# Performance work log

Hardware: AMD Instinct MI355X
Metric: run time of the kernel (lower is better)

Reference implementation:

```python
import jax, jax.numpy as jnp
import numpy as np

SEQ, BS, IN, HID, RANK = 512, 64, 1024, 1024, 256

def _xavier(key, shape):
    fan_in, fan_out = shape[0], shape[1]
    a = jnp.sqrt(6.0 / (fan_in + fan_out))
    return jax.random.uniform(key, shape, jnp.float32, -a, a)

def setup_inputs() -> dict:
    key = jax.random.key(0)
    ks = jax.random.split(key, 17)
    d = {"x": jax.random.normal(ks[0], (SEQ, BS, IN), jnp.float32)}
    names = ["ii", "hi", "if_", "hf", "ig", "hg", "io", "ho"]
    for i, n in enumerate(names):
        in_dim = IN if n[0] == "i" else HID
        d[f"W_{n}U"] = _xavier(ks[1 + 2 * i], (in_dim, RANK))
        d[f"W_{n}V"] = _xavier(ks[2 + 2 * i], (RANK, HID))
    d["b_i"] = jnp.zeros((HID,), jnp.float32)
    d["b_f"] = jnp.zeros((HID,), jnp.float32)
    d["b_g"] = jnp.zeros((HID,), jnp.float32)
    d["b_o"] = jnp.zeros((HID,), jnp.float32)
    return d

def reference(x, W_iiU, W_iiV, W_hiU, W_hiV, W_if_U, W_if_V, W_hfU, W_hfV,
              W_igU, W_igV, W_hgU, W_hgV, W_ioU, W_ioV, W_hoU, W_hoV,
              b_i, b_f, b_g, b_o):
    # Precompute input-side low-rank projections across all timesteps: (S,B,H)
    xi = (x @ W_iiU) @ W_iiV
    xf = (x @ W_if_U) @ W_if_V
    xg = (x @ W_igU) @ W_igV
    xo = (x @ W_ioU) @ W_ioV

    h0 = jnp.zeros((x.shape[1], b_i.shape[0]), x.dtype)
    c0 = jnp.zeros_like(h0)

    def step(carry, ins):
        h, c = carry
        xi_t, xf_t, xg_t, xo_t = ins
        i_t = jax.nn.sigmoid(xi_t + (h @ W_hiU) @ W_hiV + b_i)
        f_t = jax.nn.sigmoid(xf_t + (h @ W_hfU) @ W_hfV + b_f)
        g_t = jnp.tanh(xg_t + (h @ W_hgU) @ W_hgV + b_g)
        o_t = jax.nn.sigmoid(xo_t + (h @ W_hoU) @ W_hoV + b_o)
        c_n = f_t * c + i_t * g_t
        h_n = o_t * jnp.tanh(c_n)
        return (h_n, c_n), h_n

    (h_T, c_T), hidden_seq = jax.lax.scan(step, (h0, c0), (xi, xf, xg, xo))
    return hidden_seq, h_T, c_T
```

## Files before the change

### kernel.cpp

```cpp
#include <hip/hip_runtime.h>
#include <hip/hip_bf16.h>
#include <stdint.h>


typedef __attribute__((ext_vector_type(8))) short short8;
typedef __attribute__((ext_vector_type(4))) float f32x4;

#define MFMA16(a, b, c) __builtin_amdgcn_mfma_f32_16x16x32_bf16((a), (b), (c), 0, 0, 0)

__device__ inline unsigned short f2bf(float f) {
  union { float f; unsigned int u; } v; v.f = f;
  unsigned int r = v.u + 0x7fffu + ((v.u >> 16) & 1u);
  return (unsigned short)(r >> 16);
}
__device__ inline float bf2f(unsigned short u) {
  union { unsigned int u; float f; } v; v.u = ((unsigned int)u) << 16; return v.f;
}
__device__ inline float sigmoidf_(float x) {
  return 1.f / (1.f + __expf(-x));
}
__device__ inline float tanhf_(float x) {
  float cx = fminf(fmaxf(x, -15.f), 15.f);
  float e = __expf(2.f * cx);
  return (e - 1.f) / (e + 1.f);
}


__global__ __launch_bounds__(256) void convert_f32_bf16(
    const float* __restrict__ src, unsigned short* __restrict__ dst, int n) {
  int i = (blockIdx.x * 256 + threadIdx.x) * 4;
  if (i < n) {
    float4 v = *(const float4*)&src[i];
    ushort4 o;
    o.x = f2bf(v.x); o.y = f2bf(v.y); o.z = f2bf(v.z); o.w = f2bf(v.w);
    *(ushort4*)&dst[i] = o;
  }
}

__global__ __launch_bounds__(256) void transpose_f32_bf16(
    const float* __restrict__ src, unsigned short* __restrict__ dst, int R, int C) {
  int idx = blockIdx.x * 256 + threadIdx.x;
  if (idx < R * C) {
    int r = idx / C, c = idx - r * C;
    dst[(size_t)c * R + r] = f2bf(src[idx]);
  }
}


template <bool AF32>
__device__ inline short8 load_a8(const void* A, size_t row, int K, int k) {
  if constexpr (AF32) {
    const float* a = (const float*)A + row * (size_t)K + k;
    float4 f0 = *(const float4*)a;
    float4 f1 = *(const float4*)(a + 4);
    short8 r;
    r[0] = (short)f2bf(f0.x); r[1] = (short)f2bf(f0.y);
    r[2] = (short)f2bf(f0.z); r[3] = (short)f2bf(f0.w);
    r[4] = (short)f2bf(f1.x); r[5] = (short)f2bf(f1.y);
    r[6] = (short)f2bf(f1.z); r[7] = (short)f2bf(f1.w);
    return r;
  } else {
    return *(const short8*)((const unsigned short*)A + row * (size_t)K + k);
  }
}

template <bool AF32>
__global__ __launch_bounds__(256) void gemm_bf16(
    const void* __restrict__ A, const unsigned short* __restrict__ BT,
    unsigned short* __restrict__ C, int M, int N, int K,
    int ldc, int cstride, int coff) {
  __shared__ unsigned short As[128 * 64];
  __shared__ unsigned short Bs[128 * 64];

  const int tid = threadIdx.x;
  const int m0 = blockIdx.y * 128;
  const int n0 = blockIdx.x * 128;
  const int w = tid >> 6, l = tid & 63;
  const int wm = w >> 1, wn = w & 1;
  const int lr = l & 15, lk = (l >> 4) * 8;

  const int srow = tid >> 3;
  const int sseg = (tid & 7) * 8;

  f32x4 acc[4][4] = {};

  short8 av[4], bv[4];
#pragma unroll
  for (int p = 0; p < 4; ++p) {
    av[p] = load_a8<AF32>(A, m0 + p * 32 + srow, K, sseg);
    bv[p] = *(const short8*)(BT + (size_t)(n0 + p * 32 + srow) * K + sseg);
  }

  for (int k0 = 0; k0 < K; k0 += 64) {
    __syncthreads();
#pragma unroll
    for (int p = 0; p < 4; ++p) {
      *(short8*)&As[(p * 32 + srow) * 64 + sseg] = av[p];
      *(short8*)&Bs[(p * 32 + srow) * 64 + sseg] = bv[p];
    }
    __syncthreads();
    if (k0 + 64 < K) {
#pragma unroll
      for (int p = 0; p < 4; ++p) {
        av[p] = load_a8<AF32>(A, m0 + p * 32 + srow, K, k0 + 64 + sseg);
        bv[p] = *(const short8*)(BT + (size_t)(n0 + p * 32 + srow) * K + k0 + 64 + sseg);
      }
    }
#pragma unroll
    for (int kk = 0; kk < 2; ++kk) {
      const int ko = kk * 32 + lk;
      short8 a[4], b[4];
#pragma unroll
      for (int i = 0; i < 4; ++i)
        a[i] = *(const short8*)&As[(wm * 64 + i * 16 + lr) * 64 + ko];
#pragma unroll
      for (int j = 0; j < 4; ++j)
        b[j] = *(const short8*)&Bs[(wn * 64 + j * 16 + lr) * 64 + ko];
#pragma unroll
      for (int i = 0; i < 4; ++i)
#pragma unroll
        for (int j = 0; j < 4; ++j)
          acc[i][j] = MFMA16(a[i], b[j], acc[i][j]);
    }
  }

#pragma unroll
  for (int i = 0; i < 4; ++i) {
#pragma unroll
    for (int j = 0; j < 4; ++j) {
      const int rb = m0 + wm * 64 + i * 16 + (l >> 4) * 4;
      const int cb = n0 + wn * 64 + j * 16 + lr;
#pragma unroll
      for (int r = 0; r < 4; ++r)
        C[(size_t)(rb + r) * ldc + (size_t)cb * cstride + coff] = f2bf(acc[i][j][r]);
    }
  }
}


__global__ __launch_bounds__(256) void lstm_step(
    const unsigned short* __restrict__ Wrt,
    const unsigned short* __restrict__ xp_t,
    const unsigned short* __restrict__ hprev,
    unsigned short* __restrict__ hnext,
    const float* __restrict__ bi, const float* __restrict__ bf_,
    const float* __restrict__ bg, const float* __restrict__ bo,
    float* __restrict__ cstate,
    float* __restrict__ out_h,
    float* __restrict__ out_hT, float* __restrict__ out_cT,
    int t) {
  __shared__ float pre[64 * 64];

  const int tid = threadIdx.x;
  const int w = tid >> 6, l = tid & 63;
  const int c0 = blockIdx.x * 64;
  const int mr = (w >> 1) * 32;
  const int nc = c0 + (w & 1) * 32;
  const int lr = l & 15, lk = (l >> 4) * 8;

  f32x4 acc[2][2] = {};

  if (t > 0) {
#pragma unroll 2
    for (int k = 0; k < 1024; k += 32) {
      short8 a0 = *(const short8*)&hprev[(mr + lr) * 1024 + k + lk];
      short8 a1 = *(const short8*)&hprev[(mr + 16 + lr) * 1024 + k + lk];
      short8 b0 = *(const short8*)&Wrt[(size_t)(nc + lr) * 1024 + k + lk];
      short8 b1 = *(const short8*)&Wrt[(size_t)(nc + 16 + lr) * 1024 + k + lk];
      acc[0][0] = MFMA16(a0, b0, acc[0][0]);
      acc[0][1] = MFMA16(a0, b1, acc[0][1]);
      acc[1][0] = MFMA16(a1, b0, acc[1][0]);
      acc[1][1] = MFMA16(a1, b1, acc[1][1]);
    }
  }

#pragma unroll
  for (int i = 0; i < 2; ++i)
#pragma unroll
    for (int j = 0; j < 2; ++j)
#pragma unroll
      for (int r = 0; r < 4; ++r)
        pre[(mr + i * 16 + (l >> 4) * 4 + r) * 64 + (w & 1) * 32 + j * 16 + lr] =
            acc[i][j][r];
  __syncthreads();

#pragma unroll
  for (int rep = 0; rep < 4; ++rep) {
    const int cell = rep * 256 + tid;
    const int bb = cell >> 4;
    const int hh = cell & 15;
    const int hid = (c0 >> 2) + hh;

    float4 p = *(const float4*)&pre[bb * 64 + hh * 4];
    ushort4 xq = *(const ushort4*)&xp_t[bb * 4096 + c0 + hh * 4];

    float pi = p.x + bf2f(xq.x) + bi[hid];
    float pf = p.y + bf2f(xq.y) + bf_[hid];
    float pg = p.z + bf2f(xq.z) + bg[hid];
    float po = p.w + bf2f(xq.w) + bo[hid];

    float ig = sigmoidf_(pi);
    float fg = sigmoidf_(pf);
    float gg = tanhf_(pg);
    float og = sigmoidf_(po);

    float cold = (t == 0) ? 0.f : cstate[bb * 1024 + hid];
    float cn = fg * cold + ig * gg;
    float hn = og * tanhf_(cn);

    cstate[bb * 1024 + hid] = cn;
    out_h[bb * 1024 + hid] = hn;
    hnext[bb * 1024 + hid] = f2bf(hn);
    if (t == 511) {
      out_hT[bb * 1024 + hid] = hn;
      out_cT[bb * 1024 + hid] = cn;
    }
  }
}


extern "C" void kernel_launch(void* const* d_in, const int* in_sizes, int n_in,
                              void* d_out, int out_size, void* d_ws, size_t ws_size,
                              hipStream_t stream) {
  const float* x = (const float*)d_in[0];
  const float* WU[8]; const float* WV[8];
  for (int i = 0; i < 8; ++i) {
    WU[i] = (const float*)d_in[1 + 2 * i];
    WV[i] = (const float*)d_in[2 + 2 * i];
  }
  const int IGATE[4] = {0, 2, 4, 6};
  const int HGATE[4] = {1, 3, 5, 7};
  const float* bi = (const float*)d_in[17];
  const float* bf_ = (const float*)d_in[18];
  const float* bg = (const float*)d_in[19];
  const float* bo = (const float*)d_in[20];

  char* ws = (char*)d_ws;
  const size_t OFF_UTI = 0;
  const size_t OFF_VTI = OFF_UTI + 2097152;
  const size_t OFF_UBH = OFF_VTI + 2097152;
  const size_t OFF_VTH = OFF_UBH + 2097152;
  const size_t OFF_P   = OFF_VTH + 2097152;
  const size_t OFF_XP  = OFF_P + 16777216;
  const size_t OFF_WRT = OFF_XP + 268435456;
  const size_t OFF_HPP = OFF_WRT + 8388608;
  const size_t OFF_CST = OFF_HPP + 262144;

  unsigned short* uti = (unsigned short*)(ws + OFF_UTI);
  unsigned short* vti = (unsigned short*)(ws + OFF_VTI);
  unsigned short* ubh = (unsigned short*)(ws + OFF_UBH);
  unsigned short* vth = (unsigned short*)(ws + OFF_VTH);
  unsigned short* pbuf = (unsigned short*)(ws + OFF_P);
  unsigned short* xp = (unsigned short*)(ws + OFF_XP);
  unsigned short* wrt = (unsigned short*)(ws + OFF_WRT);
  unsigned short* hpp = (unsigned short*)(ws + OFF_HPP);
  float* cst = (float*)(ws + OFF_CST);
  float* out = (float*)d_out;

  for (int g = 0; g < 4; ++g) {
    transpose_f32_bf16<<<1024, 256, 0, stream>>>(WU[IGATE[g]], uti + g * 262144, 1024, 256);
    transpose_f32_bf16<<<1024, 256, 0, stream>>>(WV[IGATE[g]], vti + g * 262144, 256, 1024);
    convert_f32_bf16<<<256, 256, 0, stream>>>(WU[HGATE[g]], ubh + g * 262144, 262144);
    transpose_f32_bf16<<<1024, 256, 0, stream>>>(WV[HGATE[g]], vth + g * 262144, 256, 1024);
  }

  for (int g = 0; g < 4; ++g) {
    gemm_bf16<false><<<dim3(8, 8), 256, 0, stream>>>(
        vth + g * 262144, ubh + g * 262144, wrt,
        1024, 1024, 256, 4096, 1, g * 1024);
  }

  for (int g = 0; g < 4; ++g) {
    gemm_bf16<true><<<dim3(2, 256), 256, 0, stream>>>(
        x, uti + g * 262144, pbuf, 32768, 256, 1024, 256, 1, 0);
    gemm_bf16<false><<<dim3(8, 256), 256, 0, stream>>>(
        pbuf, vti + g * 262144, xp, 32768, 1024, 256, 4096, 4, g);
  }

  for (int t = 0; t < 512; ++t) {
    const unsigned short* hp = hpp + ((t & 1) ^ 1) * 65536;
    unsigned short* hn = hpp + (t & 1) * 65536;
    lstm_step<<<64, 256, 0, stream>>>(
        wrt, xp + (size_t)t * 262144, hp, hn,
        bi, bf_, bg, bo, cst,
        out + (size_t)t * 65536,
        out + 33554432, out + 33554432 + 65536, t);
  }
}
```

Baseline: 10.89 ms.

## Replace per-timestep LSTM launches with persistent kernel and grid barrier

Swaps the 512 per-step kernel launches for a single persistent kernel of 256 workgroups that loops over time and syncs through an atomic grid-wide barrier. Each workgroup keeps its slice of the recurrent weight matrix in registers, and the cell state stays in registers instead of going through global memory. The four waves split the K dimension and combine partial sums in shared memory. The goal is to remove launch overhead and the repeated weight reloads. In exchange, correctness depends on all 256 workgroups being resident at the same time, and the spin-wait barrier adds latency to every step.

```diff
diff --git a/kernel.cpp b/kernel.cpp
--- a/kernel.cpp
+++ b/kernel.cpp
@@ -45,6 +45,8 @@
     dst[(size_t)c * R + r] = f2bf(src[idx]);
   }
 }
+
+__global__ void zero_u32(unsigned int* p) { *p = 0u; }
 
 
 template <bool AF32>
@@ -138,83 +140,98 @@
 }
 
 
-__global__ __launch_bounds__(256) void lstm_step(
+#define NWG 256
+
+__global__ __launch_bounds__(256) void lstm_persistent(
     const unsigned short* __restrict__ Wrt,
-    const unsigned short* __restrict__ xp_t,
-    const unsigned short* __restrict__ hprev,
-    unsigned short* __restrict__ hnext,
+    const unsigned short* __restrict__ xp,
+    unsigned short* __restrict__ hpp,
     const float* __restrict__ bi, const float* __restrict__ bf_,
     const float* __restrict__ bg, const float* __restrict__ bo,
-    float* __restrict__ cstate,
-    float* __restrict__ out_h,
-    float* __restrict__ out_hT, float* __restrict__ out_cT,
-    int t) {
-  __shared__ float pre[64 * 64];
+    float* __restrict__ out,
+    unsigned int* __restrict__ bar) {
+  __shared__ float part[4][64][17];
 
   const int tid = threadIdx.x;
-  const int w = tid >> 6, l = tid & 63;
-  const int c0 = blockIdx.x * 64;
-  const int mr = (w >> 1) * 32;
-  const int nc = c0 + (w & 1) * 32;
-  const int lr = l & 15, lk = (l >> 4) * 8;
-
-  f32x4 acc[2][2] = {};
-
-  if (t > 0) {
-#pragma unroll 2
-    for (int k = 0; k < 1024; k += 32) {
-      short8 a0 = *(const short8*)&hprev[(mr + lr) * 1024 + k + lk];
-      short8 a1 = *(const short8*)&hprev[(mr + 16 + lr) * 1024 + k + lk];
-      short8 b0 = *(const short8*)&Wrt[(size_t)(nc + lr) * 1024 + k + lk];
-      short8 b1 = *(const short8*)&Wrt[(size_t)(nc + 16 + lr) * 1024 + k + lk];
-      acc[0][0] = MFMA16(a0, b0, acc[0][0]);
-      acc[0][1] = MFMA16(a0, b1, acc[0][1]);
-      acc[1][0] = MFMA16(a1, b0, acc[1][0]);
-      acc[1][1] = MFMA16(a1, b1, acc[1][1]);
-    }
-  }
-
-#pragma unroll
-  for (int i = 0; i < 2; ++i)
-#pragma unroll
-    for (int j = 0; j < 2; ++j)
+  const int w = tid >> 6;
+  const int l = tid & 63;
+  const int lr = l & 15;
+  const int lk = (l >> 4) * 8;
+  const int c0 = blockIdx.x * 16;
+  const int kbase = w * 256;
+
+  short8 bfrag[8];
+#pragma unroll
+  for (int kk = 0; kk < 8; ++kk)
+    bfrag[kk] = *(const short8*)&Wrt[(size_t)(c0 + lr) * 1024 + kbase + kk * 32 + lk];
+
+  const int bb = tid >> 2;
+  const int hh = tid & 3;
+  const int hid = (c0 >> 2) + hh;
+  const float vbi = bi[hid], vbf = bf_[hid], vbg = bg[hid], vbo = bo[hid];
+
+  float c_reg = 0.f;
+
+  for (int t = 0; t < 512; ++t) {
+    ushort4 xq = *(const ushort4*)&xp[(size_t)t * 262144 + bb * 4096 + c0 + hh * 4];
+
+    f32x4 acc[4] = {};
+    if (t > 0) {
+      const unsigned short* hprev = hpp + ((t & 1) ^ 1) * 65536;
+#pragma unroll
+      for (int kk = 0; kk < 8; ++kk) {
+        const int ko = kbase + kk * 32 + lk;
+        short8 a0 = *(const short8*)&hprev[(lr) * 1024 + ko];
+        short8 a1 = *(const short8*)&hprev[(16 + lr) * 1024 + ko];
+        short8 a2 = *(const short8*)&hprev[(32 + lr) * 1024 + ko];
+        short8 a3 = *(const short8*)&hprev[(48 + lr) * 1024 + ko];
+        acc[0] = MFMA16(a0, bfrag[kk], acc[0]);
+        acc[1] = MFMA16(a1, bfrag[kk], acc[1]);
+        acc[2] = MFMA16(a2, bfrag[kk], acc[2]);
+        acc[3] = MFMA16(a3, bfrag[kk], acc[3]);
+      }
+    }
+
+#pragma unroll
+    for (int i = 0; i < 4; ++i)
 #pragma unroll
       for (int r = 0; r < 4; ++r)
-        pre[(mr + i * 16 + (l >> 4) * 4 + r) * 64 + (w & 1) * 32 + j * 16 + lr] =
-            acc[i][j][r];
-  __syncthreads();
-
-#pragma unroll
-  for (int rep = 0; rep < 4; ++rep) {
-    const int cell = rep * 256 + tid;
-    const int bb = cell >> 4;
-    const int hh = cell & 15;
-    const int hid = (c0 >> 2) + hh;
-
-    float4 p = *(const float4*)&pre[bb * 64 + hh * 4];
-    ushort4 xq = *(const ushort4*)&xp_t[bb * 4096 + c0 + hh * 4];
-
-    float pi = p.x + bf2f(xq.x) + bi[hid];
-    float pf = p.y + bf2f(xq.y) + bf_[hid];
-    float pg = p.z + bf2f(xq.z) + bg[hid];
-    float po = p.w + bf2f(xq.w) + bo[hid];
-
-    float ig = sigmoidf_(pi);
-    float fg = sigmoidf_(pf);
-    float gg = tanhf_(pg);
-    float og = sigmoidf_(po);
-
-    float cold = (t == 0) ? 0.f : cstate[bb * 1024 + hid];
-    float cn = fg * cold + ig * gg;
-    float hn = og * tanhf_(cn);
-
-    cstate[bb * 1024 + hid] = cn;
-    out_h[bb * 1024 + hid] = hn;
-    hnext[bb * 1024 + hid] = f2bf(hn);
+        part[w][i * 16 + (l >> 4) * 4 + r][lr] = acc[i][r];
+    __syncthreads();
+
+    const int cb = hh * 4;
+    float s0 = 0.f, s1 = 0.f, s2 = 0.f, s3 = 0.f;
+#pragma unroll
+    for (int w2 = 0; w2 < 4; ++w2) {
+      s0 += part[w2][bb][cb + 0];
+      s1 += part[w2][bb][cb + 1];
+      s2 += part[w2][bb][cb + 2];
+      s3 += part[w2][bb][cb + 3];
+    }
+    float ig = sigmoidf_(s0 + bf2f(xq.x) + vbi);
+    float fg = sigmoidf_(s1 + bf2f(xq.y) + vbf);
+    float gg = tanhf_   (s2 + bf2f(xq.z) + vbg);
+    float og = sigmoidf_(s3 + bf2f(xq.w) + vbo);
+
+    c_reg = fg * c_reg + ig * gg;
+    float hn = og * tanhf_(c_reg);
+
+    out[(size_t)t * 65536 + bb * 1024 + hid] = hn;
+    hpp[(t & 1) * 65536 + bb * 1024 + hid] = f2bf(hn);
     if (t == 511) {
-      out_hT[bb * 1024 + hid] = hn;
-      out_cT[bb * 1024 + hid] = cn;
-    }
+      out[33554432 + bb * 1024 + hid] = hn;
+      out[33554432 + 65536 + bb * 1024 + hid] = c_reg;
+    }
+
+    __syncthreads();
+    if (tid == 0) {
+      __hip_atomic_fetch_add(bar, 1u, __ATOMIC_RELEASE, __HIP_MEMORY_SCOPE_AGENT);
+      const unsigned int target = (unsigned int)(t + 1) * NWG;
+      while (__hip_atomic_load(bar, __ATOMIC_RELAXED, __HIP_MEMORY_SCOPE_AGENT) < target)
+        __builtin_amdgcn_s_sleep(1);
+      __builtin_amdgcn_fence(__ATOMIC_ACQUIRE, "agent");
+    }
+    __syncthreads();
   }
 }
 
@@ -244,7 +261,7 @@
   const size_t OFF_XP  = OFF_P + 16777216;
   const size_t OFF_WRT = OFF_XP + 268435456;
   const size_t OFF_HPP = OFF_WRT + 8388608;
-  const size_t OFF_CST = OFF_HPP + 262144;
+  const size_t OFF_BAR = OFF_HPP + 262144;
 
   unsigned short* uti = (unsigned short*)(ws + OFF_UTI);
   unsigned short* vti = (unsigned short*)(ws + OFF_VTI);
@@ -254,8 +271,10 @@
   unsigned short* xp = (unsigned short*)(ws + OFF_XP);
   unsigned short* wrt = (unsigned short*)(ws + OFF_WRT);
   unsigned short* hpp = (unsigned short*)(ws + OFF_HPP);
-  float* cst = (float*)(ws + OFF_CST);
+  unsigned int* bar = (unsigned int*)(ws + OFF_BAR);
   float* out = (float*)d_out;
+
+  zero_u32<<<1, 1, 0, stream>>>(bar);
 
   for (int g = 0; g < 4; ++g) {
     transpose_f32_bf16<<<1024, 256, 0, stream>>>(WU[IGATE[g]], uti + g * 262144, 1024, 256);
@@ -277,13 +296,6 @@
         pbuf, vti + g * 262144, xp, 32768, 1024, 256, 4096, 4, g);
   }
 
-  for (int t = 0; t < 512; ++t) {
-    const unsigned short* hp = hpp + ((t & 1) ^ 1) * 65536;
-    unsigned short* hn = hpp + (t & 1) * 65536;
-    lstm_step<<<64, 256, 0, stream>>>(
-        wrt, xp + (size_t)t * 262144, hp, hn,
-        bi, bf_, bg, bo, cst,
-        out + (size_t)t * 65536,
-        out + 33554432, out + 33554432 + 65536, t);
-  }
-}
+  lstm_persistent<<<NWG, 256, 0, stream>>>(
+      wrt, xp, hpp, bi, bf_, bg, bo, out, bar);
+}
```

Result: no change. 10.94 ms (+0.5%).
